# Optimization experiments

Measured on AMD Instinct MI355X. Metric: run time of the kernel, lower is better.

Reference implementation:

```python
import jax, jax.numpy as jnp
import numpy as np

D_IN = 768
D_OUT = 768
N_HEADS = 12
HEAD_DIM = D_OUT // N_HEADS


def setup_inputs() -> dict:
    key = jax.random.key(0)
    ks = jax.random.split(key, 6)
    B, S = 2, 4096
    x = jax.random.normal(ks[0], (B, S, D_IN), dtype=jnp.float32)
    s = 0.02
    Wq = jax.random.normal(ks[1], (D_IN, D_OUT), dtype=jnp.float32) * s
    Wk = jax.random.normal(ks[2], (D_IN, D_OUT), dtype=jnp.float32) * s
    Wv = jax.random.normal(ks[3], (D_IN, D_OUT), dtype=jnp.float32) * s
    Wo = jax.random.normal(ks[4], (D_OUT, D_OUT), dtype=jnp.float32) * s
    bo = jnp.zeros((D_OUT,), dtype=jnp.float32)
    return {"x": x, "Wq": Wq, "Wk": Wk, "Wv": Wv, "Wo": Wo, "bo": bo}


def reference(x, Wq, Wk, Wv, Wo, bo):
    B, S, _ = x.shape
    # QKV projections (no bias), reshape to [B, H, S, Dh]
    q = (x @ Wq).reshape(B, S, N_HEADS, HEAD_DIM).transpose(0, 2, 1, 3)
    k = (x @ Wk).reshape(B, S, N_HEADS, HEAD_DIM).transpose(0, 2, 1, 3)
    v = (x @ Wv).reshape(B, S, N_HEADS, HEAD_DIM).transpose(0, 2, 1, 3)
    # scores: [B, H, S, S], causal mask, scaled softmax
    scores = jnp.einsum('bhqd,bhkd->bhqk', q, k)
    causal = jnp.triu(jnp.ones((S, S), dtype=bool), k=1)
    scores = jnp.where(causal, -jnp.inf, scores)
    attn = jax.nn.softmax(scores / np.sqrt(HEAD_DIM).astype(np.float32), axis=-1)
    # dropout p=0.0 -> identity
    ctx = jnp.einsum('bhqk,bhkd->bqhd', attn, v).reshape(B, S, D_OUT)
    return ctx @ Wo + bo
```

## Files before the change

kernel.cpp:

```cpp
#include <hip/hip_runtime.h>

#define S 4096
#define BATCH 2
#define D 768
#define NH 12
#define DH 64
#define NROWS (BATCH * S)
#define N_ITEMS (32 * NH * BATCH)
#define CTR_OFF 67633152

typedef __attribute__((ext_vector_type(8))) short bf16x8;
typedef __attribute__((ext_vector_type(4))) float f32x4;

__device__ __forceinline__ unsigned short f2bf(float f) {
    unsigned u = __builtin_bit_cast(unsigned, f);
    u += 0x7fff + ((u >> 16) & 1);
    return (unsigned short)(u >> 16);
}

__device__ __forceinline__ float fexp2(float x) {
#if __has_builtin(__builtin_amdgcn_exp2f)
    return __builtin_amdgcn_exp2f(x);
#else
    return exp2f(x);
#endif
}

#define GLDS16(g, l)                                                   \
    __builtin_amdgcn_global_load_lds(                                  \
        (const __attribute__((address_space(1))) void*)(g),            \
        (__attribute__((address_space(3))) void*)(l), 16, 0, 0)

__global__ __launch_bounds__(256) void cvt_x(const float* __restrict__ x,
                                             unsigned short* __restrict__ xb)
{
    int i = (blockIdx.x * 256 + threadIdx.x) * 4;
    float4 v = *(const float4*)(x + i);
    ushort4 o = make_ushort4(f2bf(v.x), f2bf(v.y), f2bf(v.z), f2bf(v.w));
    *(ushort4*)(xb + i) = o;
}

__global__ __launch_bounds__(256) void cvt_w(
    const float* __restrict__ Wq, const float* __restrict__ Wk,
    const float* __restrict__ Wv, const float* __restrict__ Wo,
    unsigned short* __restrict__ wt)
{
    __shared__ float tile[32][33];
    const int z = blockIdx.z;
    const float* W = (z == 0) ? Wq : (z == 1) ? Wk : (z == 2) ? Wv : Wo;
    const int k0 = blockIdx.x * 32, n0 = blockIdx.y * 32;
    const int t = threadIdx.x;
    const int r = t >> 3, c4 = (t & 7) * 4;

    float4 v = *(const float4*)(W + (size_t)(k0 + r) * D + n0 + c4);
    tile[r][c4 + 0] = v.x; tile[r][c4 + 1] = v.y;
    tile[r][c4 + 2] = v.z; tile[r][c4 + 3] = v.w;
    __syncthreads();
    ushort4 o = make_ushort4(f2bf(tile[c4 + 0][r]), f2bf(tile[c4 + 1][r]),
                             f2bf(tile[c4 + 2][r]), f2bf(tile[c4 + 3][r]));
    *(ushort4*)(wt + ((size_t)z * D + n0 + r) * D + k0 + c4) = o;
}

__global__ __launch_bounds__(256) void gemm_qkv(
    const unsigned short* __restrict__ xb,
    const unsigned short* __restrict__ wt,
    unsigned short* __restrict__ qb, unsigned short* __restrict__ kb,
    unsigned short* __restrict__ vtb)
{
    __shared__ unsigned short As[128 * 64];
    __shared__ unsigned short Bs[128 * 64];

    const int t = threadIdx.x;
    const int lane = t & 63, w = t >> 6;
    const int l16 = lane & 15, quad = lane >> 4;
    const int wm = w & 1, wn = w >> 1;
    const int m0 = blockIdx.x * 128;
    const int n0g = blockIdx.y * 128;
    const int z = n0g / 768;
    const int c0 = n0g - z * 768;
    const unsigned short* Wz = wt + (size_t)z * D * D;

    f32x4 acc[4][4] = {};

    for (int k0 = 0; k0 < D; k0 += 64) {
#pragma unroll
        for (int i = 0; i < 4; ++i) {
            int g = i * 256 + w * 64 + lane;
            int row = g >> 3, cl = g & 7, cg = cl ^ (row & 7);
            GLDS16(xb + (size_t)(m0 + row) * D + k0 + cg * 8,
                   As + (size_t)(i * 256 + w * 64) * 8);
            GLDS16(Wz + (size_t)(c0 + row) * D + k0 + cg * 8,
                   Bs + (size_t)(i * 256 + w * 64) * 8);
        }
        __syncthreads();
#pragma unroll
        for (int kk = 0; kk < 2; ++kk) {
            bf16x8 af[4], bf_[4];
#pragma unroll
            for (int mt = 0; mt < 4; ++mt) {
                int r = wm * 64 + mt * 16 + l16;
                int c = kk * 4 + quad;
                af[mt] = *(const bf16x8*)&As[(r * 8 + (c ^ (r & 7))) * 8];
            }
#pragma unroll
            for (int nt = 0; nt < 4; ++nt) {
                int r = wn * 64 + nt * 16 + l16;
                int c = kk * 4 + quad;
                bf_[nt] = *(const bf16x8*)&Bs[(r * 8 + (c ^ (r & 7))) * 8];
            }
#pragma unroll
            for (int mt = 0; mt < 4; ++mt)
#pragma unroll
                for (int nt = 0; nt < 4; ++nt)
                    acc[mt][nt] = __builtin_amdgcn_mfma_f32_16x16x32_bf16(
                        af[mt], bf_[nt], acc[mt][nt], 0, 0, 0);
        }
        __syncthreads();
    }

    if (z < 2) {
        unsigned short* outp = (z == 0) ? qb : kb;
        const float scale = (z == 0) ? 0.18033688011112042f : 1.0f;
#pragma unroll
        for (int mt = 0; mt < 4; ++mt) {
#pragma unroll
            for (int reg = 0; reg < 4; ++reg) {
                int m = wm * 64 + mt * 16 + quad * 4 + reg;
                int ng = m0 + m;
                int b = ng >> 12, s = ng & 4095;
#pragma unroll
                for (int nt = 0; nt < 4; ++nt) {
                    int n = c0 + wn * 64 + nt * 16 + l16;
                    int h = n >> 6, dh = n & 63;
                    outp[(((size_t)b * NH + h) * S + s) * DH + dh] =
                        f2bf(acc[mt][nt][reg] * scale);
                }
            }
        }
    } else {
#pragma unroll
        for (int mt = 0; mt < 4; ++mt) {
#pragma unroll
            for (int nt = 0; nt < 4; ++nt) {
                int m = wm * 64 + mt * 16 + quad * 4;
                int ng = m0 + m;
                int b = ng >> 12, s = ng & 4095;
                int n = c0 + wn * 64 + nt * 16 + l16;
                int h = n >> 6, dh = n & 63;
                ushort4 p = make_ushort4(
                    f2bf(acc[mt][nt][0]), f2bf(acc[mt][nt][1]),
                    f2bf(acc[mt][nt][2]), f2bf(acc[mt][nt][3]));
                *(ushort4*)(vtb + (((size_t)b * NH + h) * DH + dh) * S + s) = p;
            }
        }
    }
}

__global__ __launch_bounds__(256) void attn_mfma(
    const unsigned short* __restrict__ qg,
    const unsigned short* __restrict__ kg,
    const unsigned short* __restrict__ vtg,
    unsigned short* __restrict__ ctxb,
    int* __restrict__ work_ctr)
{
    __shared__ unsigned short Ks[2][64 * 64];
    __shared__ unsigned short Vs[2][64 * 64];
    __shared__ unsigned short Ps[4][32][64];
    __shared__ int s_item;

    const float INF = __builtin_inff();
    const int t = threadIdx.x;
    const int w = t >> 6, lane = t & 63;
    const int l16 = lane & 15, quad = lane >> 4;
    const int a7 = l16 & 7;
    const int sg = w * 64 + lane;

    for (;;) {
        if (t == 0) s_item = atomicAdd(work_ctr, 1);
        __syncthreads();
        const int p = s_item;
        if (p >= N_ITEMS) return;

        const int qt = 31 - (p / (NH * BATCH));
        const int hb = p % (NH * BATCH);
        const int h = hb % NH, b = hb / NH;
        const size_t hbase = ((size_t)b * NH + h) * (size_t)S * DH;
        const unsigned short* kp = kg + hbase;
        const unsigned short* vp = vtg + hbase;

        bf16x8 bq[2][2];
#pragma unroll
        for (int qs = 0; qs < 2; ++qs) {
            int qrow = qt * 128 + w * 32 + qs * 16 + l16;
#pragma unroll
            for (int kk = 0; kk < 2; ++kk)
                bq[qs][kk] = *(const bf16x8*)(qg + hbase + (size_t)qrow * DH +
                                              kk * 32 + quad * 8);
        }

        f32x4 acc_o[2][4] = {};
        float lsum[2] = {0.f, 0.f};

        const int jmax = 2 * qt + 1, jd = 2 * qt;

#pragma unroll
        for (int i = 0; i < 2; ++i) {
            int g = i * 256 + sg;
            int row = g >> 3, cl = g & 7, cg = cl ^ (row & 7);
            GLDS16(kp + (size_t)row * DH + cg * 8,
                   &Ks[0][(size_t)(i * 256 + w * 64) * 8]);
            GLDS16(vp + (size_t)row * S + cg * 8,
                   &Vs[0][(size_t)(i * 256 + w * 64) * 8]);
        }

        for (int j = 0; j <= jmax; ++j) {
            const int cur = j & 1;
            __syncthreads();
            if (j < jmax) {
#pragma unroll
                for (int i = 0; i < 2; ++i) {
                    int g = i * 256 + sg;
                    int row = g >> 3, cl = g & 7, cg = cl ^ (row & 7);
                    GLDS16(kp + (size_t)((j + 1) * 64 + row) * DH + cg * 8,
                           &Ks[cur ^ 1][(size_t)(i * 256 + w * 64) * 8]);
                    GLDS16(vp + (size_t)row * S + (j + 1) * 64 + cg * 8,
                           &Vs[cur ^ 1][(size_t)(i * 256 + w * 64) * 8]);
                }
            }

            const unsigned short* Kc = Ks[cur];
            const unsigned short* Vc = Vs[cur];

            f32x4 acc_s[2][4] = {};
#pragma unroll
            for (int kk = 0; kk < 2; ++kk)
#pragma unroll
                for (int ms = 0; ms < 4; ++ms) {
                    int r = ms * 16 + l16, c = kk * 4 + quad;
                    bf16x8 ak = *(const bf16x8*)&Kc[(r * 8 + (c ^ a7)) * 8];
#pragma unroll
                    for (int qs = 0; qs < 2; ++qs)
                        acc_s[qs][ms] = __builtin_amdgcn_mfma_f32_16x16x32_bf16(
                            ak, bq[qs][kk], acc_s[qs][ms], 0, 0, 0);
                }

            if (j >= jd) {
#pragma unroll
                for (int qs = 0; qs < 2; ++qs) {
                    int qrow_g = qt * 128 + w * 32 + qs * 16 + l16;
#pragma unroll
                    for (int ms = 0; ms < 4; ++ms)
#pragma unroll
                        for (int reg = 0; reg < 4; ++reg)
                            if ((j * 64 + ms * 16 + quad * 4 + reg) > qrow_g)
                                acc_s[qs][ms][reg] = -INF;
                }
            }

#pragma unroll
            for (int qs = 0; qs < 2; ++qs) {
#pragma unroll
                for (int ms = 0; ms < 4; ++ms) {
                    float e0 = fexp2(acc_s[qs][ms][0]);
                    float e1 = fexp2(acc_s[qs][ms][1]);
                    float e2 = fexp2(acc_s[qs][ms][2]);
                    float e3 = fexp2(acc_s[qs][ms][3]);
                    lsum[qs] += (e0 + e1) + (e2 + e3);
                    unsigned u01 = __builtin_amdgcn_perm(
                        __builtin_bit_cast(unsigned, e1),
                        __builtin_bit_cast(unsigned, e0), 0x07060302u);
                    unsigned u23 = __builtin_amdgcn_perm(
                        __builtin_bit_cast(unsigned, e3),
                        __builtin_bit_cast(unsigned, e2), 0x07060302u);
                    int c8 = ms * 2 + (quad >> 1);
                    *(uint2*)&Ps[w][qs * 16 + l16]
                               [(c8 ^ a7) * 8 + (quad & 1) * 4] =
                        make_uint2(u01, u23);
                }
            }

#pragma unroll
            for (int kk = 0; kk < 2; ++kk) {
                bf16x8 bp[2];
#pragma unroll
                for (int qs = 0; qs < 2; ++qs)
                    bp[qs] = *(const bf16x8*)&Ps[w][qs * 16 + l16]
                                                [((kk * 4 + quad) ^ a7) * 8];
#pragma unroll
                for (int d = 0; d < 4; ++d) {
                    int r = d * 16 + l16, c = kk * 4 + quad;
                    bf16x8 av = *(const bf16x8*)&Vc[(r * 8 + (c ^ a7)) * 8];
#pragma unroll
                    for (int qs = 0; qs < 2; ++qs)
                        acc_o[qs][d] = __builtin_amdgcn_mfma_f32_16x16x32_bf16(
                            av, bp[qs], acc_o[qs][d], 0, 0, 0);
                }
            }
        }

#pragma unroll
        for (int qs = 0; qs < 2; ++qs) {
            float tot = lsum[qs];
            tot += __shfl_xor(tot, 16);
            tot += __shfl_xor(tot, 32);
            float inv = 1.f / tot;
            lsum[qs] = 0.f;
            int qrow = qt * 128 + w * 32 + qs * 16 + l16;
            size_t base = ((size_t)(b * S + qrow)) * D + h * 64;
#pragma unroll
            for (int d = 0; d < 4; ++d) {
                ushort4 o;
                o.x = f2bf(acc_o[qs][d][0] * inv);
                o.y = f2bf(acc_o[qs][d][1] * inv);
                o.z = f2bf(acc_o[qs][d][2] * inv);
                o.w = f2bf(acc_o[qs][d][3] * inv);
                *(ushort4*)(ctxb + base + d * 16 + quad * 4) = o;
            }
        }
    }
}

__global__ __launch_bounds__(256) void gemm_out(
    const unsigned short* __restrict__ ctxb,
    const unsigned short* __restrict__ wt,
    const float* __restrict__ bo,
    float* __restrict__ out)
{
    __shared__ unsigned short As[128 * 64];
    __shared__ unsigned short Bs[128 * 64];

    const int t = threadIdx.x;
    const int lane = t & 63, w = t >> 6;
    const int l16 = lane & 15, quad = lane >> 4;
    const int wm = w & 1, wn = w >> 1;
    const int m0 = blockIdx.x * 128;
    const int n0 = blockIdx.y * 128;
    const unsigned short* Wz = wt + (size_t)3 * D * D;

    f32x4 acc[4][4] = {};

    for (int k0 = 0; k0 < D; k0 += 64) {
#pragma unroll
        for (int i = 0; i < 4; ++i) {
            int g = i * 256 + w * 64 + lane;
            int row = g >> 3, cl = g & 7, cg = cl ^ (row & 7);
            GLDS16(ctxb + (size_t)(m0 + row) * D + k0 + cg * 8,
                   As + (size_t)(i * 256 + w * 64) * 8);
            GLDS16(Wz + (size_t)(n0 + row) * D + k0 + cg * 8,
                   Bs + (size_t)(i * 256 + w * 64) * 8);
        }
        __syncthreads();
#pragma unroll
        for (int kk = 0; kk < 2; ++kk) {
            bf16x8 af[4], bf_[4];
#pragma unroll
            for (int mt = 0; mt < 4; ++mt) {
                int r = wm * 64 + mt * 16 + l16;
                int c = kk * 4 + quad;
                af[mt] = *(const bf16x8*)&As[(r * 8 + (c ^ (r & 7))) * 8];
            }
#pragma unroll
            for (int nt = 0; nt < 4; ++nt) {
                int r = wn * 64 + nt * 16 + l16;
                int c = kk * 4 + quad;
                bf_[nt] = *(const bf16x8*)&Bs[(r * 8 + (c ^ (r & 7))) * 8];
            }
#pragma unroll
            for (int mt = 0; mt < 4; ++mt)
#pragma unroll
                for (int nt = 0; nt < 4; ++nt)
                    acc[mt][nt] = __builtin_amdgcn_mfma_f32_16x16x32_bf16(
                        af[mt], bf_[nt], acc[mt][nt], 0, 0, 0);
        }
        __syncthreads();
    }

    float bv[4];
#pragma unroll
    for (int nt = 0; nt < 4; ++nt)
        bv[nt] = bo[n0 + wn * 64 + nt * 16 + l16];
#pragma unroll
    for (int mt = 0; mt < 4; ++mt)
#pragma unroll
        for (int reg = 0; reg < 4; ++reg) {
            int m = m0 + wm * 64 + mt * 16 + quad * 4 + reg;
#pragma unroll
            for (int nt = 0; nt < 4; ++nt)
                out[(size_t)m * D + n0 + wn * 64 + nt * 16 + l16] =
                    acc[mt][nt][reg] + bv[nt];
        }
}

extern "C" void kernel_launch(void* const* d_in, const int* in_sizes, int n_in,
                              void* d_out, int out_size, void* d_ws, size_t ws_size,
                              hipStream_t stream)
{
    const float* x  = (const float*)d_in[0];
    const float* Wq = (const float*)d_in[1];
    const float* Wk = (const float*)d_in[2];
    const float* Wv = (const float*)d_in[3];
    const float* Wo = (const float*)d_in[4];
    const float* bo = (const float*)d_in[5];
    float* out = (float*)d_out;

    const size_t elems = (size_t)NROWS * D;
    unsigned short* xb   = (unsigned short*)d_ws;
    unsigned short* wt   = xb + elems;
    unsigned short* q    = wt + (size_t)4 * D * D;
    unsigned short* k    = q + elems;
    unsigned short* vt   = k + elems;
    unsigned short* ctxb = vt + elems;
    int* work_ctr = (int*)((char*)d_ws + CTR_OFF);

    hipMemsetAsync(work_ctr, 0, sizeof(int), stream);

    cvt_x<<<NROWS * D / 1024, 256, 0, stream>>>(x, xb);
    dim3 gw(D / 32, D / 32, 4);
    cvt_w<<<gw, 256, 0, stream>>>(Wq, Wk, Wv, Wo, wt);

    dim3 g1(NROWS / 128, (3 * D) / 128);
    gemm_qkv<<<g1, 256, 0, stream>>>(xb, wt, q, k, vt);

    attn_mfma<<<512, 256, 0, stream>>>(q, k, vt, ctxb, work_ctr);

    dim3 g3(NROWS / 128, D / 128);
    gemm_out<<<g3, 256, 0, stream>>>(ctxb, wt, bo, out);
}
```

Baseline: 256.3 us.

## Keep softmax P in registers via permlane swaps, raise occupancy and MFMA priority

The attention kernel no longer stages the exponentiated scores through a per-wave LDS buffer. It packs them to bf16 with v_cvt_pk_bf16_f32 and rearranges them across lanes with permlane32/permlane16 swaps, so they are directly in the B-operand layout for the PV MFMA. This removes LDS writes and reads and frees LDS, which allows a 3-blocks-per-CU launch bound and a persistent grid of 768 instead of 512. s_setprio raises wave priority around the MFMA sections. The catch is the lane-permutation mapping, which must match the previous LDS layout exactly, plus added register pressure under the tighter launch bound.

New measurement: 260.7 us. No clear change (+1.7%).

```diff
diff --git a/kernel.cpp b/kernel.cpp
--- a/kernel.cpp
+++ b/kernel.cpp
@@ -11,6 +11,7 @@
 
 typedef __attribute__((ext_vector_type(8))) short bf16x8;
 typedef __attribute__((ext_vector_type(4))) float f32x4;
+typedef __attribute__((ext_vector_type(2))) unsigned uint32x2;
 
 __device__ __forceinline__ unsigned short f2bf(float f) {
     unsigned u = __builtin_bit_cast(unsigned, f);
@@ -156,7 +157,7 @@
     }
 }
 
-__global__ __launch_bounds__(256) void attn_mfma(
+__global__ __launch_bounds__(256, 3) void attn_mfma(
     const unsigned short* __restrict__ qg,
     const unsigned short* __restrict__ kg,
     const unsigned short* __restrict__ vtg,
@@ -165,7 +166,6 @@
 {
     __shared__ unsigned short Ks[2][64 * 64];
     __shared__ unsigned short Vs[2][64 * 64];
-    __shared__ unsigned short Ps[4][32][64];
     __shared__ int s_item;
 
     const float INF = __builtin_inff();
@@ -232,6 +232,7 @@
             const unsigned short* Vc = Vs[cur];
 
             f32x4 acc_s[2][4] = {};
+            __builtin_amdgcn_s_setprio(1);
 #pragma unroll
             for (int kk = 0; kk < 2; ++kk)
 #pragma unroll
@@ -243,6 +244,7 @@
                         acc_s[qs][ms] = __builtin_amdgcn_mfma_f32_16x16x32_bf16(
                             ak, bq[qs][kk], acc_s[qs][ms], 0, 0, 0);
                 }
+            __builtin_amdgcn_s_setprio(0);
 
             if (j >= jd) {
 #pragma unroll
@@ -257,8 +259,10 @@
                 }
             }
 
+            bf16x8 bp[2][2];
 #pragma unroll
             for (int qs = 0; qs < 2; ++qs) {
+                unsigned ulo[4], uhi[4];
 #pragma unroll
                 for (int ms = 0; ms < 4; ++ms) {
                     float e0 = fexp2(acc_s[qs][ms][0]);
@@ -266,26 +270,31 @@
                     float e2 = fexp2(acc_s[qs][ms][2]);
                     float e3 = fexp2(acc_s[qs][ms][3]);
                     lsum[qs] += (e0 + e1) + (e2 + e3);
-                    unsigned u01 = __builtin_amdgcn_perm(
-                        __builtin_bit_cast(unsigned, e1),
-                        __builtin_bit_cast(unsigned, e0), 0x07060302u);
-                    unsigned u23 = __builtin_amdgcn_perm(
-                        __builtin_bit_cast(unsigned, e3),
-                        __builtin_bit_cast(unsigned, e2), 0x07060302u);
-                    int c8 = ms * 2 + (quad >> 1);
-                    *(uint2*)&Ps[w][qs * 16 + l16]
-                               [(c8 ^ a7) * 8 + (quad & 1) * 4] =
-                        make_uint2(u01, u23);
-                }
-            }
-
+                    asm("v_cvt_pk_bf16_f32 %0, %1, %2"
+                        : "=v"(ulo[ms]) : "v"(e0), "v"(e1));
+                    asm("v_cvt_pk_bf16_f32 %0, %1, %2"
+                        : "=v"(uhi[ms]) : "v"(e2), "v"(e3));
+                }
+#pragma unroll
+                for (int kp2 = 0; kp2 < 2; ++kp2) {
+                    uint32x2 lo = __builtin_amdgcn_permlane32_swap(
+                        ulo[2 * kp2], ulo[2 * kp2 + 1], false, false);
+                    uint32x2 s02 = __builtin_amdgcn_permlane16_swap(
+                        lo[0], lo[1], false, false);
+                    uint32x2 hi = __builtin_amdgcn_permlane32_swap(
+                        uhi[2 * kp2], uhi[2 * kp2 + 1], false, false);
+                    uint32x2 s13 = __builtin_amdgcn_permlane16_swap(
+                        hi[0], hi[1], false, false);
+                    union { unsigned u[4]; bf16x8 v; } pb;
+                    pb.u[0] = s02[0]; pb.u[1] = s13[0];
+                    pb.u[2] = s02[1]; pb.u[3] = s13[1];
+                    bp[qs][kp2] = pb.v;
+                }
+            }
+
+            __builtin_amdgcn_s_setprio(1);
 #pragma unroll
             for (int kk = 0; kk < 2; ++kk) {
-                bf16x8 bp[2];
-#pragma unroll
-                for (int qs = 0; qs < 2; ++qs)
-                    bp[qs] = *(const bf16x8*)&Ps[w][qs * 16 + l16]
-                                                [((kk * 4 + quad) ^ a7) * 8];
 #pragma unroll
                 for (int d = 0; d < 4; ++d) {
                     int r = d * 16 + l16, c = kk * 4 + quad;
@@ -293,9 +302,10 @@
 #pragma unroll
                     for (int qs = 0; qs < 2; ++qs)
                         acc_o[qs][d] = __builtin_amdgcn_mfma_f32_16x16x32_bf16(
-                            av, bp[qs], acc_o[qs][d], 0, 0, 0);
-                }
-            }
+                            av, bp[qs][kk], acc_o[qs][d], 0, 0, 0);
+                }
+            }
+            __builtin_amdgcn_s_setprio(0);
         }
 
 #pragma unroll
@@ -421,7 +431,7 @@
     dim3 g1(NROWS / 128, (3 * D) / 128);
     gemm_qkv<<<g1, 256, 0, stream>>>(xb, wt, q, k, vt);
 
-    attn_mfma<<<512, 256, 0, stream>>>(q, k, vt, ctxb, work_ctr);
+    attn_mfma<<<768, 256, 0, stream>>>(q, k, vt, ctxb, work_ctr);
 
     dim3 g3(NROWS / 128, D / 128);
     gemm_out<<<g3, 256, 0, stream>>>(ctxb, wt, bo, out);
```
